# Kernel tuning notes

Hardware: AMD Instinct MI355X
Metric: run time of the kernel (lower is better)

Reference implementation:

```python
import jax, jax.numpy as jnp
import numpy as np

N = 50000      # nodes
E = 600000     # edges (avg degree 12)
F_IN = 64      # raw node features
HID = 128      # hidden_size
HEADS = 8
DH = HID // HEADS  # 16, per-head dim = out_channels
C = 10         # classes
L = 3          # num_gnn_layers


def setup_inputs() -> dict:
    key = jax.random.key(0)
    ks = jax.random.split(key, 12)
    g = lambda k, shape, fan: jax.random.normal(k, shape, jnp.float32) / np.float32(np.sqrt(fan))
    return {
        "x": jax.random.normal(ks[0], (N, F_IN), jnp.float32),
        "edge_index": jax.random.randint(ks[1], (2, E), 0, N, dtype=jnp.int32),
        "distance": jax.random.uniform(ks[2], (E, 1), jnp.float32),
        "Wq": g(ks[3], (L, HID, HID), HID), "bq": jnp.zeros((L, HID), jnp.float32),
        "Wk": g(ks[4], (L, HID, HID), HID), "bk": jnp.zeros((L, HID), jnp.float32),
        "Wv": g(ks[5], (L, HID, HID), HID), "bv": jnp.zeros((L, HID), jnp.float32),
        "We": g(ks[6], (L, 1, HID), 1),
        "Ws": g(ks[7], (L, HID, HID), HID), "bs": jnp.zeros((L, HID), jnp.float32),
        "ln_g": jnp.ones((L, HID), jnp.float32), "ln_b": jnp.zeros((L, HID), jnp.float32),
        "W_before": g(ks[8], (F_IN, HID), F_IN), "b_before": jnp.zeros((HID,), jnp.float32),
        "W_after": g(ks[9], (HID, C), HID), "b_after": jnp.zeros((C,), jnp.float32),
    }


def _layer_norm(h, gamma, beta):
    m = h.mean(-1, keepdims=True)
    v = ((h - m) ** 2).mean(-1, keepdims=True)
    return (h - m) * jax.lax.rsqrt(v + 1e-5) * gamma + beta


def _transformer_conv(h, src, dst, ea, Wq, bq, Wk, bk, Wv, bv, We, Ws, bs):
    # PyG TransformerConv (concat=True, beta=False, root_weight=True), eval mode (no dropout)
    q = (h @ Wq + bq).reshape(-1, HEADS, DH)   # [N,H,D]
    k = (h @ Wk + bk).reshape(-1, HEADS, DH)
    v = (h @ Wv + bv).reshape(-1, HEADS, DH)
    e = (ea @ We).reshape(-1, HEADS, DH)       # [E,H,D] edge embedding (no bias)
    ke = k[src] + e                            # gather keys along edges
    alpha = (q[dst] * ke).sum(-1) / np.float32(np.sqrt(DH))  # [E,H]
    # segment softmax over incoming edges per destination node
    amax = jax.ops.segment_max(alpha, dst, num_segments=N)
    amax = jnp.where(jnp.isfinite(amax), amax, 0.0)
    ex = jnp.exp(alpha - amax[dst])
    den = jax.ops.segment_sum(ex, dst, num_segments=N)
    a = ex / (den[dst] + 1e-16)                # [E,H]
    msg = (v[src] + e) * a[..., None]          # weighted values
    out = jax.ops.segment_sum(msg, dst, num_segments=N).reshape(-1, HEADS * DH)
    return out + h @ Ws + bs                   # root/skip connection


def reference(x, edge_index, distance, Wq, bq, Wk, bk, Wv, bv, We, Ws, bs,
              ln_g, ln_b, W_before, b_before, W_after, b_after):
    src, dst = edge_index[0], edge_index[1]
    h = jax.nn.relu(x @ W_before + b_before)   # fcnn_before
    for i in range(L):
        h = _transformer_conv(h, src, dst, distance,
                              Wq[i], bq[i], Wk[i], bk[i], Wv[i], bv[i],
                              We[i], Ws[i], bs[i])
        if i < L - 1:
            h = jax.nn.relu(_layer_norm(h, ln_g[i], ln_b[i]))
    # fcnn_after
    h = jax.nn.relu(_layer_norm(h, ln_g[L - 1], ln_b[L - 1]))
    h = h @ W_after + b_after
    return jax.nn.log_softmax(h, axis=1)
```

## Files before the change

### kernel.cpp

```cpp
#include <hip/hip_runtime.h>
#include <cstdint>
#include <cstddef>

#define NN 50000
#define NE 600000
#define FIN 64
#define HID 128
#define NCLS 10
#define NLAYER 3

#define QSCALE 0.36067376022224085f

typedef __bf16 bf16x8 __attribute__((ext_vector_type(8)));
typedef float f32x4 __attribute__((ext_vector_type(4)));
typedef float f32x2 __attribute__((ext_vector_type(2)));

__device__ __forceinline__ unsigned short f2bf(float f) {
    unsigned int u = __builtin_bit_cast(unsigned int, f);
    u += 0x7fffu + ((u >> 16) & 1u);
    return (unsigned short)(u >> 16);
}
__device__ __forceinline__ float bf2f(unsigned short s) {
    unsigned int u = ((unsigned int)s) << 16;
    return __builtin_bit_cast(float, u);
}

__global__ __launch_bounds__(256) void k_prep(
    const float* __restrict__ Wq, const float* __restrict__ Wk,
    const float* __restrict__ Wv, const float* __restrict__ Ws,
    const float* __restrict__ Wbe, const float* __restrict__ Waf,
    unsigned short* __restrict__ Wt12,
    unsigned short* __restrict__ Wbt,
    float* __restrict__ Wat,
    const int* __restrict__ edst, int* __restrict__ counts)
{
    int blk = blockIdx.x;
    int tid = threadIdx.x;
    if (blk < 768) {
        int m = blk >> 6;
        int l = m >> 2, which = m & 3;
        const float* src;
        if (which == 0) src = Wq; else if (which == 1) src = Wk;
        else if (which == 2) src = Wv; else src = Ws;
        src += (size_t)l * HID * HID;
        int idx = (blk & 63) * 256 + tid;
        int c = idx >> 7, k = idx & 127;
        Wt12[(size_t)m * 16384 + (size_t)c * 128 + k] = f2bf(src[(size_t)k * 128 + c]);
    } else if (blk < 800) {
        int idx = (blk - 768) * 256 + tid;
        int c = idx >> 6, k = idx & 63;
        Wbt[(size_t)c * 64 + k] = f2bf(Wbe[(size_t)k * 128 + c]);
    } else if (blk < 805) {
        int i = (blk - 800) * 256 + tid;
        if (i < 1280) {
            int c = i >> 7, f = i & 127;
            Wat[i] = Waf[f * 10 + c];
        }
    } else {
        int e = (blk - 805) * 256 + tid;
        if (e < NE) atomicAdd(&counts[edst[e]], 1);
    }
}

__global__ __launch_bounds__(512) void k_scan1(const int* __restrict__ counts,
                                               int* __restrict__ row_ptr,
                                               int* __restrict__ partials, int n) {
    __shared__ int sm[512];
    int tid = threadIdx.x;
    int i = blockIdx.x * 512 + tid;
    int v = (i < n) ? counts[i] : 0;
    sm[tid] = v;
    __syncthreads();
    #pragma unroll
    for (int off = 1; off < 512; off <<= 1) {
        int t = (tid >= off) ? sm[tid - off] : 0;
        __syncthreads();
        sm[tid] += t;
        __syncthreads();
    }
    if (i < n) row_ptr[i] = sm[tid] - v;
    if (tid == 511) partials[blockIdx.x] = sm[511];
}

__global__ __launch_bounds__(128) void k_scan2(int* __restrict__ partials, int nb) {
    __shared__ int sm[128];
    int t = threadIdx.x;
    int v = (t < nb) ? partials[t] : 0;
    sm[t] = v;
    __syncthreads();
    #pragma unroll
    for (int off = 1; off < 128; off <<= 1) {
        int x = (t >= off) ? sm[t - off] : 0;
        __syncthreads();
        sm[t] += x;
        __syncthreads();
    }
    if (t < nb) partials[t] = sm[t] - v;
}

__global__ __launch_bounds__(512) void k_scan3(int* __restrict__ row_ptr,
                                               const int* __restrict__ partials, int n) {
    int i = blockIdx.x * 512 + threadIdx.x;
    if (i < n) row_ptr[i] += partials[blockIdx.x];
}

__global__ __launch_bounds__(256) void k_fill(const int* __restrict__ esrc,
                                              const int* __restrict__ edst,
                                              const float* __restrict__ dist,
                                              int* __restrict__ cursor,
                                              const int* __restrict__ row_ptr,
                                              int2* __restrict__ srcd) {
    int e = blockIdx.x * 256 + threadIdx.x;
    if (e < NE) {
        int d = edst[e];
        int pos = atomicAdd(&cursor[d], 1);
        srcd[row_ptr[d] + pos] = make_int2(esrc[e], __float_as_int(dist[e]));
    }
}

__global__ __launch_bounds__(512) void k_qkvs(
    const unsigned short* __restrict__ Ab, int nrows,
    const unsigned short* __restrict__ Wt,
    const float* __restrict__ bq, const float* __restrict__ bk,
    const float* __restrict__ bv, const float* __restrict__ bs,
    unsigned short* __restrict__ qb,
    unsigned char* __restrict__ kv8,
    unsigned short* __restrict__ hsb)
{
    const int tid = threadIdx.x;
    const int w = tid >> 6, lane = tid & 63;
    const int m = w >> 1, ch = w & 1;
    const float* bias = (m == 0) ? bq : (m == 1) ? bk : (m == 2) ? bv : bs;
    const unsigned short* Wm = Wt + (size_t)m * 16384;
    const int lc = lane & 15, lk = lane >> 4;

    bf16x8 bw[4][4];
    float4 bb[4];
    #pragma unroll
    for (int ct = 0; ct < 4; ++ct) {
        int col = ch * 64 + ct * 16 + lc;
        bb[ct] = *(const float4*)(bias + ch * 64 + ct * 16 + lk * 4);
        #pragma unroll
        for (int kb = 0; kb < 4; ++kb)
            bw[ct][kb] = *(const bf16x8*)(Wm + (size_t)col * 128 + kb * 32 + lk * 8);
    }

    const int r0 = blockIdx.x * 64;
    #pragma unroll
    for (int rt = 0; rt < 4; ++rt) {
        const int arow = r0 + rt * 16 + lc;
        const bool rv = arow < nrows;
        bf16x8 z = {};
        bf16x8 a[4];
        #pragma unroll
        for (int kb = 0; kb < 4; ++kb)
            a[kb] = rv ? *(const bf16x8*)(Ab + (size_t)arow * 128 + kb * 32 + lk * 8) : z;
        #pragma unroll
        for (int ct = 0; ct < 4; ++ct) {
            f32x4 acc = {0.f, 0.f, 0.f, 0.f};
            #pragma unroll
            for (int kb = 0; kb < 4; ++kb)
                acc = __builtin_amdgcn_mfma_f32_16x16x32_bf16(bw[ct][kb], a[kb], acc, 0, 0, 0);
            if (rv) {
                const int colb = ch * 64 + ct * 16 + lk * 4;
                float v0 = acc[0] + bb[ct].x, v1 = acc[1] + bb[ct].y;
                float v2 = acc[2] + bb[ct].z, v3 = acc[3] + bb[ct].w;
                if (m == 0) {
                    ushort4 o;
                    o.x = f2bf(v0 * QSCALE); o.y = f2bf(v1 * QSCALE);
                    o.z = f2bf(v2 * QSCALE); o.w = f2bf(v3 * QSCALE);
                    *(ushort4*)(qb + (size_t)arow * 128 + colb) = o;
                } else if (m == 1 || m == 2) {
                    unsigned int pk = __builtin_amdgcn_cvt_pk_fp8_f32(v0, v1, 0, false);
                    pk = __builtin_amdgcn_cvt_pk_fp8_f32(v2, v3, pk, true);
                    *(unsigned int*)(kv8 + (size_t)arow * 256 + (colb >> 2) * 8 + (m == 2 ? 4 : 0)) = pk;
                } else {
                    ushort4 o;
                    o.x = f2bf(v0); o.y = f2bf(v1); o.z = f2bf(v2); o.w = f2bf(v3);
                    *(ushort4*)(hsb + (size_t)arow * 128 + colb) = o;
                }
            }
        }
    }
}

__global__ __launch_bounds__(256) void k_gin(
    const float* __restrict__ x, int nrows,
    const unsigned short* __restrict__ Wt,
    const float* __restrict__ bias,
    unsigned short* __restrict__ hb)
{
    const int tid = threadIdx.x;
    const int w = tid >> 6, lane = tid & 63;
    const int lc = lane & 15, lk = lane >> 4;
    const int arow = blockIdx.x * 64 + w * 16 + lc;
    const bool rv = arow < nrows;

    bf16x8 a[2];
    #pragma unroll
    for (int kb = 0; kb < 2; ++kb) {
        union { bf16x8 v; unsigned short u[8]; } t;
        #pragma unroll
        for (int q = 0; q < 2; ++q) {
            float4 f = rv ? *(const float4*)(x + (size_t)arow * 64 + kb * 32 + lk * 8 + q * 4)
                          : make_float4(0.f, 0.f, 0.f, 0.f);
            t.u[q * 4 + 0] = f2bf(f.x); t.u[q * 4 + 1] = f2bf(f.y);
            t.u[q * 4 + 2] = f2bf(f.z); t.u[q * 4 + 3] = f2bf(f.w);
        }
        a[kb] = t.v;
    }

    #pragma unroll
    for (int ct = 0; ct < 8; ++ct) {
        f32x4 acc = {0.f, 0.f, 0.f, 0.f};
        #pragma unroll
        for (int kb = 0; kb < 2; ++kb) {
            bf16x8 bwf = *(const bf16x8*)(Wt + (size_t)(ct * 16 + lc) * 64 + kb * 32 + lk * 8);
            acc = __builtin_amdgcn_mfma_f32_16x16x32_bf16(bwf, a[kb], acc, 0, 0, 0);
        }
        if (rv) {
            float4 bv_ = *(const float4*)(bias + ct * 16 + lk * 4);
            ushort4 o;
            o.x = f2bf(fmaxf(acc[0] + bv_.x, 0.f));
            o.y = f2bf(fmaxf(acc[1] + bv_.y, 0.f));
            o.z = f2bf(fmaxf(acc[2] + bv_.z, 0.f));
            o.w = f2bf(fmaxf(acc[3] + bv_.w, 0.f));
            *(ushort4*)(hb + (size_t)arow * 128 + ct * 16 + lk * 4) = o;
        }
    }
}

#define FETCHE(t, sreg, kreg, ereg) {                                     \
    int rel_ = 2 * (t) + half;                                            \
    ereg = rel_ < cnt;                                                    \
    sreg = srcd[beg + (ereg ? rel_ : 0)];                                 \
    kreg = *(const uint2*)(kv8 + (size_t)sreg.x * 256 + l5 * 8); }

#define COMPE(sreg, kreg, ereg) {                                         \
    float dd_ = __int_as_float(sreg.y);                                   \
    f32x2 k01_ = __builtin_amdgcn_cvt_pk_f32_fp8(kreg.x, false);          \
    f32x2 k23_ = __builtin_amdgcn_cvt_pk_f32_fp8(kreg.x, true);           \
    float p_ = q0 * k01_.x + q1 * k01_.y + q2 * k23_.x + q3 * k23_.y;     \
    p_ += __shfl_xor(p_, 1);                                              \
    p_ += __shfl_xor(p_, 2);                                              \
    p_ = fmaf(dd_, qwe, p_);                                              \
    float w_ = (ereg) ? exp2f(p_) : 0.f;                                  \
    s += w_;                                                              \
    sd = fmaf(dd_, w_, sd);                                               \
    f32x2 v01_ = __builtin_amdgcn_cvt_pk_f32_fp8(kreg.y, false);          \
    f32x2 v23_ = __builtin_amdgcn_cvt_pk_f32_fp8(kreg.y, true);           \
    va0 = fmaf(v01_.x, w_, va0); va1 = fmaf(v01_.y, w_, va1);             \
    va2 = fmaf(v23_.x, w_, va2); va3 = fmaf(v23_.y, w_, va3); }

template <int LAST>
__global__ __launch_bounds__(256, 6) void k_attn(
    const unsigned short* __restrict__ qb,
    const unsigned short* __restrict__ hsb,
    const unsigned char* __restrict__ kv8,
    const int2* __restrict__ srcd,
    const float* __restrict__ We,
    const int* __restrict__ row_ptr,
    const float* __restrict__ lng,
    const float* __restrict__ lnb,
    unsigned short* __restrict__ hb,
    const float* __restrict__ Wat,
    const float* __restrict__ ba,
    float* __restrict__ out, int nnodes)
{
    const int wid = threadIdx.x >> 6;
    const int lane = threadIdx.x & 63;
    const int n = blockIdx.x * 4 + wid;
    if (n >= nnodes) return;
    const int half = lane >> 5;
    const int l5 = lane & 31;
    const int d0 = l5 * 4;

    const int beg = row_ptr[n];
    const int cnt = row_ptr[n + 1] - beg;

    ushort4 qu = *(const ushort4*)(qb + (size_t)n * 128 + d0);
    const float q0 = bf2f(qu.x), q1 = bf2f(qu.y), q2 = bf2f(qu.z), q3 = bf2f(qu.w);
    const float4 wv = *(const float4*)(We + d0);
    float qwe = q0 * wv.x + q1 * wv.y + q2 * wv.z + q3 * wv.w;
    qwe += __shfl_xor(qwe, 1);
    qwe += __shfl_xor(qwe, 2);

    float s = 0.f, sd = 0.f;
    float va0 = 0.f, va1 = 0.f, va2 = 0.f, va3 = 0.f;

    if (cnt > 0) {
        const int niter = (cnt + 1) >> 1;
        int2 sA, sB, sC;
        uint2 kA, kB, kC;
        bool eA, eB, eC;
        FETCHE(0, sA, kA, eA);
        if (1 < niter) FETCHE(1, sB, kB, eB);
        int t = 0;
        while (true) {
            if (t + 2 < niter) FETCHE(t + 2, sC, kC, eC);
            COMPE(sA, kA, eA);
            if (++t >= niter) break;
            if (t + 2 < niter) FETCHE(t + 2, sA, kA, eA);
            COMPE(sB, kB, eB);
            if (++t >= niter) break;
            if (t + 2 < niter) FETCHE(t + 2, sB, kB, eB);
            COMPE(sC, kC, eC);
            if (++t >= niter) break;
        }
    }

    s  += __shfl_xor(s, 32);
    sd += __shfl_xor(sd, 32);
    va0 += __shfl_xor(va0, 32);
    va1 += __shfl_xor(va1, 32);
    va2 += __shfl_xor(va2, 32);
    va3 += __shfl_xor(va3, 32);

    const float inv = 1.f / (s + 1e-16f);
    const ushort4 hu = *(const ushort4*)(hsb + (size_t)n * 128 + d0);
    float o0 = fmaf(fmaf(wv.x, sd, va0), inv, bf2f(hu.x));
    float o1 = fmaf(fmaf(wv.y, sd, va1), inv, bf2f(hu.y));
    float o2 = fmaf(fmaf(wv.z, sd, va2), inv, bf2f(hu.z));
    float o3 = fmaf(fmaf(wv.w, sd, va3), inv, bf2f(hu.w));

    float tt = o0 + o1 + o2 + o3;
    #pragma unroll
    for (int msk = 1; msk < 32; msk <<= 1) tt += __shfl_xor(tt, msk);
    const float mean = tt * 0.0078125f;
    const float e0 = o0 - mean, e1 = o1 - mean, e2 = o2 - mean, e3 = o3 - mean;
    float vv2 = e0 * e0 + e1 * e1 + e2 * e2 + e3 * e3;
    #pragma unroll
    for (int msk = 1; msk < 32; msk <<= 1) vv2 += __shfl_xor(vv2, msk);
    const float rstd = rsqrtf(vv2 * 0.0078125f + 1e-5f);
    const float4 g4 = *(const float4*)(lng + d0);
    const float4 b4 = *(const float4*)(lnb + d0);
    const float y0 = fmaxf(fmaf(e0 * rstd, g4.x, b4.x), 0.f);
    const float y1 = fmaxf(fmaf(e1 * rstd, g4.y, b4.y), 0.f);
    const float y2 = fmaxf(fmaf(e2 * rstd, g4.z, b4.z), 0.f);
    const float y3 = fmaxf(fmaf(e3 * rstd, g4.w, b4.w), 0.f);

    if (LAST) {
        float lg[NCLS];
        #pragma unroll
        for (int c = 0; c < NCLS; ++c) {
            float4 wa = *(const float4*)(Wat + c * 128 + d0);
            float p = y0 * wa.x + y1 * wa.y + y2 * wa.z + y3 * wa.w;
            #pragma unroll
            for (int msk = 1; msk < 32; msk <<= 1) p += __shfl_xor(p, msk);
            lg[c] = p + ba[c];
        }
        float mx = lg[0];
        #pragma unroll
        for (int c = 1; c < NCLS; ++c) mx = fmaxf(mx, lg[c]);
        float sum = 0.f;
        #pragma unroll
        for (int c = 0; c < NCLS; ++c) sum += __expf(lg[c] - mx);
        float lse = mx + __logf(sum);
        if (lane == 0) {
            #pragma unroll
            for (int c = 0; c < NCLS; ++c) out[(size_t)n * NCLS + c] = lg[c] - lse;
        }
    } else if (lane < 32) {
        ushort4 o;
        o.x = f2bf(y0); o.y = f2bf(y1); o.z = f2bf(y2); o.w = f2bf(y3);
        *(ushort4*)(hb + (size_t)n * 128 + d0) = o;
    }
}

extern "C" void kernel_launch(void* const* d_in, const int* in_sizes, int n_in,
                              void* d_out, int out_size, void* d_ws, size_t ws_size,
                              hipStream_t stream)
{
    const float* x    = (const float*)d_in[0];
    const int*   ei   = (const int*)d_in[1];
    const float* dist = (const float*)d_in[2];
    const float* Wq   = (const float*)d_in[3];
    const float* bq   = (const float*)d_in[4];
    const float* Wk   = (const float*)d_in[5];
    const float* bk   = (const float*)d_in[6];
    const float* Wv   = (const float*)d_in[7];
    const float* bv   = (const float*)d_in[8];
    const float* We   = (const float*)d_in[9];
    const float* Wsk  = (const float*)d_in[10];
    const float* bs   = (const float*)d_in[11];
    const float* lng  = (const float*)d_in[12];
    const float* lnb  = (const float*)d_in[13];
    const float* Wbe  = (const float*)d_in[14];
    const float* bbe  = (const float*)d_in[15];
    const float* Waf  = (const float*)d_in[16];
    const float* baf  = (const float*)d_in[17];
    float* out = (float*)d_out;
    const int* esrc = ei;
    const int* edst = ei + NE;

    char* ws = (char*)d_ws;
    size_t off = 0;
    unsigned short* qb  = (unsigned short*)(ws + off); off += 12800000;
    unsigned short* hsb = (unsigned short*)(ws + off); off += 12800000;
    unsigned char*  kv8 = (unsigned char*)(ws + off);  off += 12800000;
    unsigned short* hb  = (unsigned short*)(ws + off); off += 12800000;
    unsigned short* Wt12 = (unsigned short*)(ws + off); off += 393216;
    unsigned short* Wbt  = (unsigned short*)(ws + off); off += 16384;
    float* Wat = (float*)(ws + off);   off += 5120;
    int* counts   = (int*)(ws + off);  off += 200192;
    int* cursor   = (int*)(ws + off);  off += 200192;
    int* row_ptr  = (int*)(ws + off);  off += 200192;
    int* partials = (int*)(ws + off);  off += 512;
    int2* srcd    = (int2*)(ws + off); off += (size_t)NE * 8;

    hipMemsetAsync(counts, 0, 2 * 200192, stream);
    k_prep<<<805 + (NE + 255) / 256, 256, 0, stream>>>(
        Wq, Wk, Wv, Wsk, Wbe, Waf, Wt12, Wbt, Wat, edst, counts);
    int nsb = (NN + 1 + 511) / 512;
    k_scan1<<<nsb, 512, 0, stream>>>(counts, row_ptr, partials, NN + 1);
    k_scan2<<<1, 128, 0, stream>>>(partials, nsb);
    k_scan3<<<nsb, 512, 0, stream>>>(row_ptr, partials, NN + 1);
    k_fill<<<(NE + 255) / 256, 256, 0, stream>>>(esrc, edst, dist, cursor, row_ptr, srcd);

    const int ngb = (NN + 63) / 64;

    k_gin<<<ngb, 256, 0, stream>>>(x, NN, Wbt, bbe, hb);

    for (int l = 0; l < NLAYER; ++l) {
        const unsigned short* wt = Wt12 + (size_t)l * 4 * 16384;
        k_qkvs<<<ngb, 512, 0, stream>>>(hb, NN, wt,
            bq + l * HID, bk + l * HID, bv + l * HID, bs + l * HID,
            qb, kv8, hsb);
        const int nab = (NN + 3) / 4;
        if (l < NLAYER - 1) {
            k_attn<0><<<nab, 256, 0, stream>>>(qb, hsb, kv8, srcd, We + l * HID,
                row_ptr, lng + l * HID, lnb + l * HID, hb, nullptr, nullptr, nullptr, NN);
        } else {
            k_attn<1><<<nab, 256, 0, stream>>>(qb, hsb, kv8, srcd, We + l * HID,
                row_ptr, lng + l * HID, lnb + l * HID, hb, Wat, baf, out, NN);
        }
    }
}
```

Before: 358.9 us.

## Fuse input projection into first QKV kernel and batch edge fetches via shuffles

Merges the input linear+ReLU kernel into the first-layer QKVS projection, keeping the hidden tile in shared memory so hb is never written to or reread from global memory. The attention loop now loads up to 64 edge (src, distance) records with one coalesced load per wave, broadcasts them with shuffles, and issues eight key/value gathers at a time before computing. Edges beyond 64 per node fall back to a simple serial loop. This adds shared memory pressure and more registers in the attention kernel, which may lower occupancy.

Result: faster. 342.0 us (-4.7%).

```diff
diff --git a/kernel.cpp b/kernel.cpp
--- a/kernel.cpp
+++ b/kernel.cpp
@@ -118,6 +118,30 @@
     }
 }
 
+__device__ __forceinline__ void qkvs_store(
+    int m, int arow, int colb, f32x4 acc, float4 bb, int nrows,
+    unsigned short* __restrict__ qb, unsigned char* __restrict__ kv8,
+    unsigned short* __restrict__ hsb)
+{
+    if (arow >= nrows) return;
+    float v0 = acc[0] + bb.x, v1 = acc[1] + bb.y;
+    float v2 = acc[2] + bb.z, v3 = acc[3] + bb.w;
+    if (m == 0) {
+        ushort4 o;
+        o.x = f2bf(v0 * QSCALE); o.y = f2bf(v1 * QSCALE);
+        o.z = f2bf(v2 * QSCALE); o.w = f2bf(v3 * QSCALE);
+        *(ushort4*)(qb + (size_t)arow * 128 + colb) = o;
+    } else if (m == 1 || m == 2) {
+        unsigned int pk = __builtin_amdgcn_cvt_pk_fp8_f32(v0, v1, 0, false);
+        pk = __builtin_amdgcn_cvt_pk_fp8_f32(v2, v3, pk, true);
+        *(unsigned int*)(kv8 + (size_t)arow * 256 + (colb >> 2) * 8 + (m == 2 ? 4 : 0)) = pk;
+    } else {
+        ushort4 o;
+        o.x = f2bf(v0); o.y = f2bf(v1); o.z = f2bf(v2); o.w = f2bf(v3);
+        *(ushort4*)(hsb + (size_t)arow * 128 + colb) = o;
+    }
+}
+
 __global__ __launch_bounds__(512) void k_qkvs(
     const unsigned short* __restrict__ Ab, int nrows,
     const unsigned short* __restrict__ Wt,
@@ -161,94 +185,122 @@
             #pragma unroll
             for (int kb = 0; kb < 4; ++kb)
                 acc = __builtin_amdgcn_mfma_f32_16x16x32_bf16(bw[ct][kb], a[kb], acc, 0, 0, 0);
-            if (rv) {
-                const int colb = ch * 64 + ct * 16 + lk * 4;
-                float v0 = acc[0] + bb[ct].x, v1 = acc[1] + bb[ct].y;
-                float v2 = acc[2] + bb[ct].z, v3 = acc[3] + bb[ct].w;
-                if (m == 0) {
-                    ushort4 o;
-                    o.x = f2bf(v0 * QSCALE); o.y = f2bf(v1 * QSCALE);
-                    o.z = f2bf(v2 * QSCALE); o.w = f2bf(v3 * QSCALE);
-                    *(ushort4*)(qb + (size_t)arow * 128 + colb) = o;
-                } else if (m == 1 || m == 2) {
-                    unsigned int pk = __builtin_amdgcn_cvt_pk_fp8_f32(v0, v1, 0, false);
-                    pk = __builtin_amdgcn_cvt_pk_fp8_f32(v2, v3, pk, true);
-                    *(unsigned int*)(kv8 + (size_t)arow * 256 + (colb >> 2) * 8 + (m == 2 ? 4 : 0)) = pk;
-                } else {
-                    ushort4 o;
-                    o.x = f2bf(v0); o.y = f2bf(v1); o.z = f2bf(v2); o.w = f2bf(v3);
-                    *(ushort4*)(hsb + (size_t)arow * 128 + colb) = o;
-                }
-            }
-        }
-    }
-}
-
-__global__ __launch_bounds__(256) void k_gin(
+            qkvs_store(m, arow, ch * 64 + ct * 16 + lk * 4, acc, bb[ct], nrows, qb, kv8, hsb);
+        }
+    }
+}
+
+__global__ __launch_bounds__(512) void k_gqkvs(
     const float* __restrict__ x, int nrows,
+    const unsigned short* __restrict__ Wbt,
+    const float* __restrict__ bbe,
     const unsigned short* __restrict__ Wt,
-    const float* __restrict__ bias,
-    unsigned short* __restrict__ hb)
+    const float* __restrict__ bq, const float* __restrict__ bk,
+    const float* __restrict__ bv, const float* __restrict__ bs,
+    unsigned short* __restrict__ qb,
+    unsigned char* __restrict__ kv8,
+    unsigned short* __restrict__ hsb)
 {
+    __shared__ unsigned short hs_s[64 * 136];
     const int tid = threadIdx.x;
     const int w = tid >> 6, lane = tid & 63;
     const int lc = lane & 15, lk = lane >> 4;
-    const int arow = blockIdx.x * 64 + w * 16 + lc;
-    const bool rv = arow < nrows;
-
-    bf16x8 a[2];
-    #pragma unroll
-    for (int kb = 0; kb < 2; ++kb) {
-        union { bf16x8 v; unsigned short u[8]; } t;
-        #pragma unroll
-        for (int q = 0; q < 2; ++q) {
-            float4 f = rv ? *(const float4*)(x + (size_t)arow * 64 + kb * 32 + lk * 8 + q * 4)
-                          : make_float4(0.f, 0.f, 0.f, 0.f);
-            t.u[q * 4 + 0] = f2bf(f.x); t.u[q * 4 + 1] = f2bf(f.y);
-            t.u[q * 4 + 2] = f2bf(f.z); t.u[q * 4 + 3] = f2bf(f.w);
-        }
-        a[kb] = t.v;
-    }
-
-    #pragma unroll
-    for (int ct = 0; ct < 8; ++ct) {
-        f32x4 acc = {0.f, 0.f, 0.f, 0.f};
+    const int r0 = blockIdx.x * 64;
+
+    {
+        const int rt0 = w & 3, ch0 = w >> 2;
+        const int arl = rt0 * 16 + lc;
+        const int arow = r0 + arl;
+        const bool rv = arow < nrows;
+        bf16x8 a[2];
         #pragma unroll
         for (int kb = 0; kb < 2; ++kb) {
-            bf16x8 bwf = *(const bf16x8*)(Wt + (size_t)(ct * 16 + lc) * 64 + kb * 32 + lk * 8);
-            acc = __builtin_amdgcn_mfma_f32_16x16x32_bf16(bwf, a[kb], acc, 0, 0, 0);
-        }
-        if (rv) {
-            float4 bv_ = *(const float4*)(bias + ct * 16 + lk * 4);
+            union { bf16x8 v; unsigned short u[8]; } t;
+            #pragma unroll
+            for (int q = 0; q < 2; ++q) {
+                float4 f = rv ? *(const float4*)(x + (size_t)arow * 64 + kb * 32 + lk * 8 + q * 4)
+                              : make_float4(0.f, 0.f, 0.f, 0.f);
+                t.u[q * 4 + 0] = f2bf(f.x); t.u[q * 4 + 1] = f2bf(f.y);
+                t.u[q * 4 + 2] = f2bf(f.z); t.u[q * 4 + 3] = f2bf(f.w);
+            }
+            a[kb] = t.v;
+        }
+        #pragma unroll
+        for (int ct = 0; ct < 4; ++ct) {
+            const int col = ch0 * 64 + ct * 16 + lc;
+            f32x4 acc = {0.f, 0.f, 0.f, 0.f};
+            #pragma unroll
+            for (int kb = 0; kb < 2; ++kb) {
+                bf16x8 bwf = *(const bf16x8*)(Wbt + (size_t)col * 64 + kb * 32 + lk * 8);
+                acc = __builtin_amdgcn_mfma_f32_16x16x32_bf16(bwf, a[kb], acc, 0, 0, 0);
+            }
+            float4 bv_ = *(const float4*)(bbe + ch0 * 64 + ct * 16 + lk * 4);
             ushort4 o;
-            o.x = f2bf(fmaxf(acc[0] + bv_.x, 0.f));
-            o.y = f2bf(fmaxf(acc[1] + bv_.y, 0.f));
-            o.z = f2bf(fmaxf(acc[2] + bv_.z, 0.f));
-            o.w = f2bf(fmaxf(acc[3] + bv_.w, 0.f));
-            *(ushort4*)(hb + (size_t)arow * 128 + ct * 16 + lk * 4) = o;
-        }
-    }
-}
-
-#define FETCHE(t, sreg, kreg, ereg) {                                     \
-    int rel_ = 2 * (t) + half;                                            \
-    ereg = rel_ < cnt;                                                    \
-    sreg = srcd[beg + (ereg ? rel_ : 0)];                                 \
-    kreg = *(const uint2*)(kv8 + (size_t)sreg.x * 256 + l5 * 8); }
-
-#define COMPE(sreg, kreg, ereg) {                                         \
-    float dd_ = __int_as_float(sreg.y);                                   \
-    f32x2 k01_ = __builtin_amdgcn_cvt_pk_f32_fp8(kreg.x, false);          \
-    f32x2 k23_ = __builtin_amdgcn_cvt_pk_f32_fp8(kreg.x, true);           \
+            o.x = rv ? f2bf(fmaxf(acc[0] + bv_.x, 0.f)) : 0;
+            o.y = rv ? f2bf(fmaxf(acc[1] + bv_.y, 0.f)) : 0;
+            o.z = rv ? f2bf(fmaxf(acc[2] + bv_.z, 0.f)) : 0;
+            o.w = rv ? f2bf(fmaxf(acc[3] + bv_.w, 0.f)) : 0;
+            *(ushort4*)(hs_s + arl * 136 + ch0 * 64 + ct * 16 + lk * 4) = o;
+        }
+    }
+    __syncthreads();
+
+    const int m = w >> 1, ch = w & 1;
+    const float* bias = (m == 0) ? bq : (m == 1) ? bk : (m == 2) ? bv : bs;
+    const unsigned short* Wm = Wt + (size_t)m * 16384;
+
+    bf16x8 bw[4][4];
+    float4 bb[4];
+    #pragma unroll
+    for (int ct = 0; ct < 4; ++ct) {
+        int col = ch * 64 + ct * 16 + lc;
+        bb[ct] = *(const float4*)(bias + ch * 64 + ct * 16 + lk * 4);
+        #pragma unroll
+        for (int kb = 0; kb < 4; ++kb)
+            bw[ct][kb] = *(const bf16x8*)(Wm + (size_t)col * 128 + kb * 32 + lk * 8);
+    }
+
+    #pragma unroll
+    for (int rt = 0; rt < 4; ++rt) {
+        const int arl = rt * 16 + lc;
+        const int arow = r0 + arl;
+        bf16x8 a[4];
+        #pragma unroll
+        for (int kb = 0; kb < 4; ++kb)
+            a[kb] = *(const bf16x8*)(hs_s + arl * 136 + kb * 32 + lk * 8);
+        #pragma unroll
+        for (int ct = 0; ct < 4; ++ct) {
+            f32x4 acc = {0.f, 0.f, 0.f, 0.f};
+            #pragma unroll
+            for (int kb = 0; kb < 4; ++kb)
+                acc = __builtin_amdgcn_mfma_f32_16x16x32_bf16(bw[ct][kb], a[kb], acc, 0, 0, 0);
+            qkvs_store(m, arow, ch * 64 + ct * 16 + lk * 4, acc, bb[ct], nrows, qb, kv8, hsb);
+        }
+    }
+}
+
+#define FET(Ki, i) {                                                      \
+    int e_ = base + 2 * (i) + half;                                       \
+    int ec_ = e_ < cmax ? e_ : 0;                                         \
+    int sx_ = __shfl(sd0.x, ec_);                                         \
+    Ki = *(const uint2*)(kv8 + (size_t)sx_ * 256 + l5 * 8); }
+
+#define CMP(Ki, i) {                                                      \
+    int e_ = base + 2 * (i) + half;                                       \
+    bool val_ = e_ < cmax;                                                \
+    int ec_ = val_ ? e_ : 0;                                              \
+    float dd_ = __int_as_float(__shfl(sd0.y, ec_));                       \
+    f32x2 k01_ = __builtin_amdgcn_cvt_pk_f32_fp8(Ki.x, false);            \
+    f32x2 k23_ = __builtin_amdgcn_cvt_pk_f32_fp8(Ki.x, true);             \
     float p_ = q0 * k01_.x + q1 * k01_.y + q2 * k23_.x + q3 * k23_.y;     \
     p_ += __shfl_xor(p_, 1);                                              \
     p_ += __shfl_xor(p_, 2);                                              \
     p_ = fmaf(dd_, qwe, p_);                                              \
-    float w_ = (ereg) ? exp2f(p_) : 0.f;                                  \
+    float w_ = val_ ? exp2f(p_) : 0.f;                                    \
     s += w_;                                                              \
     sd = fmaf(dd_, w_, sd);                                               \
-    f32x2 v01_ = __builtin_amdgcn_cvt_pk_f32_fp8(kreg.y, false);          \
-    f32x2 v23_ = __builtin_amdgcn_cvt_pk_f32_fp8(kreg.y, true);           \
+    f32x2 v01_ = __builtin_amdgcn_cvt_pk_f32_fp8(Ki.y, false);            \
+    f32x2 v23_ = __builtin_amdgcn_cvt_pk_f32_fp8(Ki.y, true);             \
     va0 = fmaf(v01_.x, w_, va0); va1 = fmaf(v01_.y, w_, va1);             \
     va2 = fmaf(v23_.x, w_, va2); va3 = fmaf(v23_.y, w_, va3); }
 
@@ -289,23 +341,34 @@
     float va0 = 0.f, va1 = 0.f, va2 = 0.f, va3 = 0.f;
 
     if (cnt > 0) {
-        const int niter = (cnt + 1) >> 1;
-        int2 sA, sB, sC;
-        uint2 kA, kB, kC;
-        bool eA, eB, eC;
-        FETCHE(0, sA, kA, eA);
-        if (1 < niter) FETCHE(1, sB, kB, eB);
-        int t = 0;
-        while (true) {
-            if (t + 2 < niter) FETCHE(t + 2, sC, kC, eC);
-            COMPE(sA, kA, eA);
-            if (++t >= niter) break;
-            if (t + 2 < niter) FETCHE(t + 2, sA, kA, eA);
-            COMPE(sB, kB, eB);
-            if (++t >= niter) break;
-            if (t + 2 < niter) FETCHE(t + 2, sB, kB, eB);
-            COMPE(sC, kC, eC);
-            if (++t >= niter) break;
+        int2 sd0 = srcd[beg + (lane < cnt ? lane : 0)];
+        const int cmax = cnt < 64 ? cnt : 64;
+        const int nch = (cmax + 15) >> 4;
+        for (int ch = 0; ch < nch; ++ch) {
+            const int base = ch << 4;
+            uint2 kA, kB, kC, kD, kE, kF, kG, kH;
+            FET(kA, 0) FET(kB, 1) FET(kC, 2) FET(kD, 3)
+            FET(kE, 4) FET(kF, 5) FET(kG, 6) FET(kH, 7)
+            CMP(kA, 0) CMP(kB, 1) CMP(kC, 2) CMP(kD, 3)
+            CMP(kE, 4) CMP(kF, 5) CMP(kG, 6) CMP(kH, 7)
+        }
+        for (int e = 64 + half; e < cnt; e += 2) {
+            int2 sde = srcd[beg + e];
+            uint2 kr = *(const uint2*)(kv8 + (size_t)sde.x * 256 + l5 * 8);
+            float dd_ = __int_as_float(sde.y);
+            f32x2 k01_ = __builtin_amdgcn_cvt_pk_f32_fp8(kr.x, false);
+            f32x2 k23_ = __builtin_amdgcn_cvt_pk_f32_fp8(kr.x, true);
+            float p_ = q0 * k01_.x + q1 * k01_.y + q2 * k23_.x + q3 * k23_.y;
+            p_ += __shfl_xor(p_, 1);
+            p_ += __shfl_xor(p_, 2);
+            p_ = fmaf(dd_, qwe, p_);
+            float w_ = exp2f(p_);
+            s += w_;
+            sd = fmaf(dd_, w_, sd);
+            f32x2 v01_ = __builtin_amdgcn_cvt_pk_f32_fp8(kr.y, false);
+            f32x2 v23_ = __builtin_amdgcn_cvt_pk_f32_fp8(kr.y, true);
+            va0 = fmaf(v01_.x, w_, va0); va1 = fmaf(v01_.y, w_, va1);
+            va2 = fmaf(v23_.x, w_, va2); va3 = fmaf(v23_.y, w_, va3);
         }
     }
 
@@ -406,7 +469,7 @@
     int* cursor   = (int*)(ws + off);  off += 200192;
     int* row_ptr  = (int*)(ws + off);  off += 200192;
     int* partials = (int*)(ws + off);  off += 512;
-    int2* srcd    = (int2*)(ws + off); off += (size_t)NE * 8;
+    int2* srcd    = (int2*)(ws + off); off += (size_t)NE * 8 + 512;
 
     hipMemsetAsync(counts, 0, 2 * 200192, stream);
     k_prep<<<805 + (NE + 255) / 256, 256, 0, stream>>>(
@@ -418,15 +481,18 @@
     k_fill<<<(NE + 255) / 256, 256, 0, stream>>>(esrc, edst, dist, cursor, row_ptr, srcd);
 
     const int ngb = (NN + 63) / 64;
-
-    k_gin<<<ngb, 256, 0, stream>>>(x, NN, Wbt, bbe, hb);
+    const int nab = (NN + 3) / 4;
 
     for (int l = 0; l < NLAYER; ++l) {
         const unsigned short* wt = Wt12 + (size_t)l * 4 * 16384;
-        k_qkvs<<<ngb, 512, 0, stream>>>(hb, NN, wt,
-            bq + l * HID, bk + l * HID, bv + l * HID, bs + l * HID,
-            qb, kv8, hsb);
-        const int nab = (NN + 3) / 4;
+        if (l == 0) {
+            k_gqkvs<<<ngb, 512, 0, stream>>>(x, NN, Wbt, bbe, wt,
+                bq, bk, bv, bs, qb, kv8, hsb);
+        } else {
+            k_qkvs<<<ngb, 512, 0, stream>>>(hb, NN, wt,
+                bq + l * HID, bk + l * HID, bv + l * HID, bs + l * HID,
+                qb, kv8, hsb);
+        }
         if (l < NLAYER - 1) {
             k_attn<0><<<nab, 256, 0, stream>>>(qb, hsb, kv8, srcd, We + l * HID,
                 row_ptr, lng + l * HID, lnb + l * HID, hb, nullptr, nullptr, nullptr, NN);
```
